# Optimization experiments

Measured on AMD Instinct MI355X. Metric: run time of the kernel, lower is better.

The kernel has to match this reference:

```python
import jax, jax.numpy as jnp
import numpy as np

H = 512
B = 32
T = 2048


def setup_inputs() -> dict:
    key = jax.random.key(0)
    ks = jax.random.split(key, 8)
    hidden = jax.random.normal(ks[0], (1, B, H), dtype=jnp.float32)
    encoder_outputs = jax.random.normal(ks[1], (T, B, H), dtype=jnp.float32)
    coverage = jax.random.uniform(ks[2], (B, T), dtype=jnp.float32)
    # nn.Linear(3H, H): weight [H, 3H], bias [H]
    W_attn = jax.random.normal(ks[3], (H, 3 * H), dtype=jnp.float32) / np.sqrt(3 * H)
    b_attn = jax.random.normal(ks[4], (H,), dtype=jnp.float32) / np.sqrt(3 * H)
    # v ~ Normal(0, 1/sqrt(H))
    v = jax.random.normal(ks[5], (H,), dtype=jnp.float32) / np.sqrt(H)
    # nn.Linear(1, H, bias=False): weight [H, 1]
    W_cov = jax.random.normal(ks[6], (H, 1), dtype=jnp.float32)
    return {"hidden": hidden, "encoder_outputs": encoder_outputs, "coverage": coverage,
            "W_attn": W_attn, "b_attn": b_attn, "v": v, "W_cov": W_cov}


def reference(hidden, encoder_outputs, coverage, W_attn, b_attn, v, W_cov):
    # hidden: [1,B,H], encoder_outputs: [T,B,H], coverage: [B,T]
    enc = jnp.transpose(encoder_outputs, (1, 0, 2))          # [B,T,H]
    b, t, h = enc.shape
    hrep = jnp.broadcast_to(hidden[0][:, None, :], (b, t, h))  # [B,T,H]
    # coverage_feature = Linear(1,H,bias=False)(coverage[...,None]) -> outer product
    cov_feat = coverage[..., None] * W_cov[:, 0]               # [B,T,H]
    x = jnp.concatenate([hrep, enc, cov_feat], axis=-1)        # [B,T,3H]
    energy = jax.nn.relu(jnp.einsum('btk,hk->bth', x, W_attn) + b_attn)  # [B,T,H]
    scores = jnp.einsum('bth,h->bt', energy, v)                # [B,T]
    attn_weights = jax.nn.softmax(scores, axis=1)              # softmax over T
    coverage_new = coverage + attn_weights                     # [B,T]
    return attn_weights[:, None, :], coverage_new
```

## Files before the change

### kernel.cpp

```cpp
#include <hip/hip_runtime.h>
#include <hip/hip_bf16.h>

typedef unsigned short u16;
typedef __attribute__((ext_vector_type(8))) short bf16x8;
typedef __attribute__((ext_vector_type(4))) float f32x4;

#define T_DIM 2048
#define B_DIM 32
#define H_DIM 512
#define M_DIM (T_DIM * B_DIM)

__device__ inline unsigned pack2(float a, float b) {
  union { __hip_bfloat162 h2; unsigned u; } c;
  c.h2 = __float22bfloat162_rn(make_float2(a, b));
  return c.u;
}

__global__ __launch_bounds__(256) void prep_kernel(
    const float* __restrict__ hidden, const float* __restrict__ W_attn,
    const float* __restrict__ b_attn, const float* __restrict__ W_cov,
    u16* __restrict__ W2bf, float* __restrict__ r, float* __restrict__ u)
{
  const int tid = blockIdx.x * 256 + threadIdx.x;
  const int pair = tid >> 2;
  const int kq = tid & 3;
  const int b = pair >> 9, h = pair & 511;

  {
    const float* hid = hidden + b * 512 + kq * 128;
    const float* w1 = W_attn + (size_t)h * 1536 + kq * 128;
    float acc = 0.f;
    #pragma unroll 8
    for (int k = 0; k < 128; k += 4) {
      float4 x = *(const float4*)(hid + k);
      float4 w = *(const float4*)(w1 + k);
      acc += x.x * w.x + x.y * w.y + x.z * w.z + x.w * w.w;
    }
    acc += __shfl_xor(acc, 1);
    acc += __shfl_xor(acc, 2);
    if (kq == 0) r[pair] = acc + b_attn[h];
  }

  {
    int j0 = tid * 4;
    int hh = j0 >> 9, kk = j0 & 511;
    float4 w = *(const float4*)(W_attn + (size_t)hh * 1536 + 512 + kk);
    uint2 p;
    p.x = pack2(w.x, w.y);
    p.y = pack2(w.z, w.w);
    int f = hh >> 4, c = hh & 15;
    int ks = kk >> 5, quad = (kk >> 3) & 3, e = kk & 7;
    *(uint2*)(W2bf + (size_t)((f * 16 + ks) * 64 + quad * 16 + c) * 8 + e) = p;
  }

  if (tid < 2048) {
    int h3 = tid >> 2;
    const float* w3 = W_attn + (size_t)h3 * 1536 + 1024 + kq * 128;
    const float* wc = W_cov + kq * 128;
    float su = 0.f;
    #pragma unroll 8
    for (int k = 0; k < 128; k += 4) {
      float4 a = *(const float4*)(w3 + k);
      float4 c = *(const float4*)(wc + k);
      su += a.x * c.x + a.y * c.y + a.z * c.z + a.w * c.w;
    }
    su += __shfl_xor(su, 1);
    su += __shfl_xor(su, 2);
    if (kq == 0) u[h3] = su;
  }
}

__global__ __launch_bounds__(512, 4) void gemm_score(
    const float* __restrict__ enc, const u16* __restrict__ W2bf,
    const float* __restrict__ r, const float* __restrict__ u,
    const float* __restrict__ vv, const float* __restrict__ cov,
    float* __restrict__ part)
{
  const int m0 = blockIdx.x * 64;
  const int tid = threadIdx.x;
  const int lane = tid & 63;
  const int w = tid >> 6;
  const int quad = lane >> 4, col = lane & 15;

  __shared__ u16 As[64 * 512];

  #pragma unroll
  for (int it = 0; it < 8; ++it) {
    int un = tid + 512 * it;
    int row = un >> 6;
    int g = un & 63;
    const float* ga = enc + (size_t)(m0 + row) * 512 + g * 8;
    float4 f0 = *(const float4*)ga;
    float4 f1 = *(const float4*)(ga + 4);
    uint4 p;
    p.x = pack2(f0.x, f0.y);
    p.y = pack2(f0.z, f0.w);
    p.z = pack2(f1.x, f1.y);
    p.w = pack2(f1.z, f1.w);
    *(uint4*)&As[row * 512 + (g ^ (row & 7)) * 8] = p;
  }
  __syncthreads();

  f32x4 acc[4][4] = {};
  const u16* bbase = W2bf + (size_t)w * 32768 + lane * 8;

  bf16x8 bcur[4], bnxt[4];
  #pragma unroll
  for (int j = 0; j < 4; ++j)
    bcur[j] = *(const bf16x8*)(bbase + j * 8192);

  #pragma unroll
  for (int ks = 0; ks < 16; ++ks) {
    if (ks < 15) {
      #pragma unroll
      for (int j = 0; j < 4; ++j)
        bnxt[j] = *(const bf16x8*)(bbase + j * 8192 + (ks + 1) * 512);
    }
    bf16x8 af[4];
    #pragma unroll
    for (int i = 0; i < 4; ++i) {
      int row = i * 16 + col;
      af[i] = *(const bf16x8*)&As[row * 512 + ((ks * 4 + quad) ^ (col & 7)) * 8];
    }
    #pragma unroll
    for (int i = 0; i < 4; ++i)
      #pragma unroll
      for (int j = 0; j < 4; ++j)
        acc[i][j] = __builtin_amdgcn_mfma_f32_16x16x32_bf16(af[i], bcur[j], acc[i][j], 0, 0, 0);
    #pragma unroll
    for (int j = 0; j < 4; ++j) bcur[j] = bnxt[j];
  }

  float uj[4], vj[4];
  #pragma unroll
  for (int j = 0; j < 4; ++j) {
    int gh = w * 64 + j * 16 + col;
    uj[j] = u[gh];
    vj[j] = vv[gh];
  }
  #pragma unroll
  for (int pair = 0; pair < 2; ++pair) {
    #pragma unroll
    for (int reg = 0; reg < 4; ++reg) {
      int b = pair * 16 + quad * 4 + reg;
      const float* rb = r + b * 512;
      float rbj[4];
      #pragma unroll
      for (int j = 0; j < 4; ++j) rbj[j] = rb[w * 64 + j * 16 + col];
      #pragma unroll
      for (int isub = 0; isub < 2; ++isub) {
        int i = pair + isub * 2;
        int t = (m0 >> 5) + isub;
        float cv = cov[b * 2048 + t];
        float s = 0.f;
        #pragma unroll
        for (int j = 0; j < 4; ++j) {
          float e = acc[i][j][reg] + rbj[j] + cv * uj[j];
          e = fmaxf(e, 0.f);
          s += e * vj[j];
        }
        s += __shfl_xor(s, 1);
        s += __shfl_xor(s, 2);
        s += __shfl_xor(s, 4);
        s += __shfl_xor(s, 8);
        if (col == 0) part[(size_t)(w * 32 + b) * 2048 + t] = s;
      }
    }
  }
}

__global__ __launch_bounds__(256) void softmax_kernel(
    const float* __restrict__ part, const float* __restrict__ cov, float* __restrict__ out)
{
  const int b = blockIdx.x;
  const int tid = threadIdx.x;
  const int lane = tid & 63, wid = tid >> 6;
  __shared__ float red[4];
  float loc[8];
  float lmax = -3.4e38f;
  #pragma unroll
  for (int i = 0; i < 8; ++i) {
    int t = tid + i * 256;
    float s = 0.f;
    #pragma unroll
    for (int p = 0; p < 8; ++p) s += part[(size_t)(p * 32 + b) * 2048 + t];
    loc[i] = s;
    lmax = fmaxf(lmax, s);
  }
  #pragma unroll
  for (int o = 32; o; o >>= 1) lmax = fmaxf(lmax, __shfl_xor(lmax, o));
  if (lane == 0) red[wid] = lmax;
  __syncthreads();
  float bmax = fmaxf(fmaxf(red[0], red[1]), fmaxf(red[2], red[3]));
  __syncthreads();
  float lsum = 0.f;
  #pragma unroll
  for (int i = 0; i < 8; ++i) { loc[i] = __expf(loc[i] - bmax); lsum += loc[i]; }
  #pragma unroll
  for (int o = 32; o; o >>= 1) lsum += __shfl_xor(lsum, o);
  if (lane == 0) red[wid] = lsum;
  __syncthreads();
  float inv = 1.0f / (red[0] + red[1] + red[2] + red[3]);
  #pragma unroll
  for (int i = 0; i < 8; ++i) {
    int t = tid + i * 256;
    float a = loc[i] * inv;
    out[b * 2048 + t] = a;
    out[65536 + b * 2048 + t] = cov[b * 2048 + t] + a;
  }
}

extern "C" void kernel_launch(void* const* d_in, const int* in_sizes, int n_in,
                              void* d_out, int out_size, void* d_ws, size_t ws_size,
                              hipStream_t stream) {
  const float* hidden = (const float*)d_in[0];
  const float* enc    = (const float*)d_in[1];
  const float* cov    = (const float*)d_in[2];
  const float* W_attn = (const float*)d_in[3];
  const float* b_attn = (const float*)d_in[4];
  const float* vv     = (const float*)d_in[5];
  const float* W_cov  = (const float*)d_in[6];
  float* out = (float*)d_out;

  u16* W2bf = (u16*)d_ws;
  float* r  = (float*)((char*)d_ws + 512 * 1024);
  float* u  = r + 32 * 512;
  float* part = u + 512;

  hipLaunchKernelGGL(prep_kernel, dim3(256), dim3(256), 0, stream,
                     hidden, W_attn, b_attn, W_cov, W2bf, r, u);
  hipLaunchKernelGGL(gemm_score, dim3(1024), dim3(512), 0, stream,
                     enc, W2bf, r, u, vv, cov, part);
  hipLaunchKernelGGL(softmax_kernel, dim3(32), dim3(256), 0, stream,
                     part, cov, out);
}
```

Baseline: 273.2 us.

## Stream fp32 encoder tiles into LDS asynchronously with double-buffered K chunks

Replaces the upfront synchronous load-and-convert of the whole 64x512 A tile with async global_load_lds copies of fp32 data. The copies go into two LDS buffers of 128-wide K chunks, so loading the next chunk overlaps MFMA work on the current one. The bf16 conversion moves from the staging step to each LDS read. Every one of the 8 waves now converts the same A fragments, which adds redundant VALU packing work. It also adds three extra block barriers.

```diff
diff --git a/kernel.cpp b/kernel.cpp
--- a/kernel.cpp
+++ b/kernel.cpp
@@ -2,6 +2,7 @@
 #include <hip/hip_bf16.h>
 
 typedef unsigned short u16;
+typedef unsigned int u32;
 typedef __attribute__((ext_vector_type(8))) short bf16x8;
 typedef __attribute__((ext_vector_type(4))) float f32x4;
 
@@ -14,6 +15,11 @@
   union { __hip_bfloat162 h2; unsigned u; } c;
   c.h2 = __float22bfloat162_rn(make_float2(a, b));
   return c.u;
+}
+
+__device__ inline void gload_lds16(const float* g, float* lds) {
+  __builtin_amdgcn_global_load_lds((const __attribute__((address_space(1))) u32*)g,
+                                   (__attribute__((address_space(3))) u32*)lds, 16, 0, 0);
 }
 
 __global__ __launch_bounds__(256) void prep_kernel(
@@ -82,53 +88,67 @@
   const int w = tid >> 6;
   const int quad = lane >> 4, col = lane & 15;
 
-  __shared__ u16 As[64 * 512];
-
-  #pragma unroll
-  for (int it = 0; it < 8; ++it) {
-    int un = tid + 512 * it;
-    int row = un >> 6;
-    int g = un & 63;
-    const float* ga = enc + (size_t)(m0 + row) * 512 + g * 8;
-    float4 f0 = *(const float4*)ga;
-    float4 f1 = *(const float4*)(ga + 4);
-    uint4 p;
-    p.x = pack2(f0.x, f0.y);
-    p.y = pack2(f0.z, f0.w);
-    p.z = pack2(f1.x, f1.y);
-    p.w = pack2(f1.z, f1.w);
-    *(uint4*)&As[row * 512 + (g ^ (row & 7)) * 8] = p;
-  }
-  __syncthreads();
+  __shared__ float As[2][64 * 128];
+
+  const int srow_half = lane >> 5;
+  const int sj = lane & 31;
 
   f32x4 acc[4][4] = {};
   const u16* bbase = W2bf + (size_t)w * 32768 + lane * 8;
 
-  bf16x8 bcur[4], bnxt[4];
+  #pragma unroll
+  for (int it = 0; it < 4; ++it) {
+    int c = w * 4 + it;
+    int row = 2 * c + srow_half;
+    int g = sj ^ (row & 7);
+    gload_lds16(enc + (size_t)(m0 + row) * 512 + 0 * 128 + g * 4, &As[0][c * 256]);
+  }
+  __syncthreads();
+
+  bf16x8 bbuf[2][4];
   #pragma unroll
   for (int j = 0; j < 4; ++j)
-    bcur[j] = *(const bf16x8*)(bbase + j * 8192);
-
-  #pragma unroll
-  for (int ks = 0; ks < 16; ++ks) {
-    if (ks < 15) {
-      #pragma unroll
-      for (int j = 0; j < 4; ++j)
-        bnxt[j] = *(const bf16x8*)(bbase + j * 8192 + (ks + 1) * 512);
-    }
-    bf16x8 af[4];
+    bbuf[0][j] = *(const bf16x8*)(bbase + j * 8192);
+
+  for (int q = 0; q < 4; ++q) {
+    if (q < 3) {
+      #pragma unroll
+      for (int it = 0; it < 4; ++it) {
+        int c = w * 4 + it;
+        int row = 2 * c + srow_half;
+        int g = sj ^ (row & 7);
+        gload_lds16(enc + (size_t)(m0 + row) * 512 + (q + 1) * 128 + g * 4,
+                    &As[(q + 1) & 1][c * 256]);
+      }
+    }
+    const float* Ab = As[q & 1];
     #pragma unroll
-    for (int i = 0; i < 4; ++i) {
-      int row = i * 16 + col;
-      af[i] = *(const bf16x8*)&As[row * 512 + ((ks * 4 + quad) ^ (col & 7)) * 8];
-    }
-    #pragma unroll
-    for (int i = 0; i < 4; ++i)
-      #pragma unroll
-      for (int j = 0; j < 4; ++j)
-        acc[i][j] = __builtin_amdgcn_mfma_f32_16x16x32_bf16(af[i], bcur[j], acc[i][j], 0, 0, 0);
-    #pragma unroll
-    for (int j = 0; j < 4; ++j) bcur[j] = bnxt[j];
+    for (int ksl = 0; ksl < 4; ++ksl) {
+      int ksg = q * 4 + ksl;
+      if (ksg < 15) {
+        #pragma unroll
+        for (int j = 0; j < 4; ++j)
+          bbuf[(ksg + 1) & 1][j] = *(const bf16x8*)(bbase + j * 8192 + (ksg + 1) * 512);
+      }
+      const int gb = ksl * 8 + quad * 2;
+      #pragma unroll
+      for (int i = 0; i < 4; ++i) {
+        int row = i * 16 + col;
+        int sw = col & 7;
+        float4 d0 = *(const float4*)&Ab[row * 128 + (gb ^ sw) * 4];
+        float4 d1 = *(const float4*)&Ab[row * 128 + ((gb + 1) ^ sw) * 4];
+        uint4 pa;
+        pa.x = pack2(d0.x, d0.y);
+        pa.y = pack2(d0.z, d0.w);
+        pa.z = pack2(d1.x, d1.y);
+        pa.w = pack2(d1.z, d1.w);
+        bf16x8 af = *(bf16x8*)&pa;
+        #pragma unroll
+        for (int j = 0; j < 4; ++j)
+          acc[i][j] = __builtin_amdgcn_mfma_f32_16x16x32_bf16(af, bbuf[ksg & 1][j], acc[i][j], 0, 0, 0);
+      }
+    }
+    if (q < 3) __syncthreads();
   }
 
   float uj[4], vj[4];
@@ -139,17 +159,17 @@
     vj[j] = vv[gh];
   }
   #pragma unroll
-  for (int pair = 0; pair < 2; ++pair) {
+  for (int pr = 0; pr < 2; ++pr) {
     #pragma unroll
     for (int reg = 0; reg < 4; ++reg) {
-      int b = pair * 16 + quad * 4 + reg;
+      int b = pr * 16 + quad * 4 + reg;
       const float* rb = r + b * 512;
       float rbj[4];
       #pragma unroll
       for (int j = 0; j < 4; ++j) rbj[j] = rb[w * 64 + j * 16 + col];
       #pragma unroll
       for (int isub = 0; isub < 2; ++isub) {
-        int i = pair + isub * 2;
+        int i = pr + isub * 2;
         int t = (m0 >> 5) + isub;
         float cv = cov[b * 2048 + t];
         float s = 0.f;
```

New measurement: 290.5 us. 1.06x slower.

## Load encoder tiles directly into registers, drop LDS staging, split N across blocks

Applied to the files above, without the earlier changes.

Removes the shared-memory staging of the fp32 encoder tile: each wave now loads its A fragments straight from global memory, converts them to bf16 in registers, and double-buffers both A and B loads across k-steps. The grid is doubled, with each 256-thread block covering half of the hidden dimension, so there are more, smaller blocks. This avoids the LDS write, the barrier and the LDS reads. In exchange, every wave re-reads encoder rows that other waves and the sibling block also read, using narrow strided accesses that depend on cache hits.

```diff
diff --git a/kernel.cpp b/kernel.cpp
--- a/kernel.cpp
+++ b/kernel.cpp
@@ -2,6 +2,7 @@
 #include <hip/hip_bf16.h>
 
 typedef unsigned short u16;
+typedef unsigned int u32;
 typedef __attribute__((ext_vector_type(8))) short bf16x8;
 typedef __attribute__((ext_vector_type(4))) float f32x4;
 
@@ -70,86 +71,85 @@
   }
 }
 
-__global__ __launch_bounds__(512, 4) void gemm_score(
+__global__ __launch_bounds__(256, 3) void gemm_score(
     const float* __restrict__ enc, const u16* __restrict__ W2bf,
     const float* __restrict__ r, const float* __restrict__ u,
     const float* __restrict__ vv, const float* __restrict__ cov,
     float* __restrict__ part)
 {
-  const int m0 = blockIdx.x * 64;
+  const int p = blockIdx.x;
+  const int m0 = (p & 1023) * 64;
+  const int y = p >> 10;
   const int tid = threadIdx.x;
   const int lane = tid & 63;
   const int w = tid >> 6;
+  const int slab = y * 4 + w;
   const int quad = lane >> 4, col = lane & 15;
 
-  __shared__ u16 As[64 * 512];
-
-  #pragma unroll
-  for (int it = 0; it < 8; ++it) {
-    int un = tid + 512 * it;
-    int row = un >> 6;
-    int g = un & 63;
-    const float* ga = enc + (size_t)(m0 + row) * 512 + g * 8;
-    float4 f0 = *(const float4*)ga;
-    float4 f1 = *(const float4*)(ga + 4);
-    uint4 p;
-    p.x = pack2(f0.x, f0.y);
-    p.y = pack2(f0.z, f0.w);
-    p.z = pack2(f1.x, f1.y);
-    p.w = pack2(f1.z, f1.w);
-    *(uint4*)&As[row * 512 + (g ^ (row & 7)) * 8] = p;
-  }
-  __syncthreads();
-
   f32x4 acc[4][4] = {};
-  const u16* bbase = W2bf + (size_t)w * 32768 + lane * 8;
-
-  bf16x8 bcur[4], bnxt[4];
+  const u16* bbase = W2bf + (size_t)(slab * 4) * 8192 + lane * 8;
+  const float* abase = enc + (size_t)(m0 + col) * 512 + quad * 8;
+
+  float4 araw[8];
+  bf16x8 bbuf[2][4];
+
+  #pragma unroll
+  for (int i = 0; i < 4; ++i) {
+    araw[i * 2]     = *(const float4*)(abase + i * 8192);
+    araw[i * 2 + 1] = *(const float4*)(abase + i * 8192 + 4);
+  }
   #pragma unroll
   for (int j = 0; j < 4; ++j)
-    bcur[j] = *(const bf16x8*)(bbase + j * 8192);
+    bbuf[0][j] = *(const bf16x8*)(bbase + j * 8192);
 
   #pragma unroll
   for (int ks = 0; ks < 16; ++ks) {
+    bf16x8 af[4];
+    #pragma unroll
+    for (int i = 0; i < 4; ++i) {
+      uint4 pa;
+      pa.x = pack2(araw[i * 2].x,     araw[i * 2].y);
+      pa.y = pack2(araw[i * 2].z,     araw[i * 2].w);
+      pa.z = pack2(araw[i * 2 + 1].x, araw[i * 2 + 1].y);
+      pa.w = pack2(araw[i * 2 + 1].z, araw[i * 2 + 1].w);
+      af[i] = *(bf16x8*)&pa;
+    }
     if (ks < 15) {
       #pragma unroll
+      for (int i = 0; i < 4; ++i) {
+        araw[i * 2]     = *(const float4*)(abase + i * 8192 + (ks + 1) * 32);
+        araw[i * 2 + 1] = *(const float4*)(abase + i * 8192 + (ks + 1) * 32 + 4);
+      }
+      #pragma unroll
       for (int j = 0; j < 4; ++j)
-        bnxt[j] = *(const bf16x8*)(bbase + j * 8192 + (ks + 1) * 512);
-    }
-    bf16x8 af[4];
-    #pragma unroll
-    for (int i = 0; i < 4; ++i) {
-      int row = i * 16 + col;
-      af[i] = *(const bf16x8*)&As[row * 512 + ((ks * 4 + quad) ^ (col & 7)) * 8];
+        bbuf[(ks + 1) & 1][j] = *(const bf16x8*)(bbase + j * 8192 + (ks + 1) * 512);
     }
     #pragma unroll
     for (int i = 0; i < 4; ++i)
       #pragma unroll
       for (int j = 0; j < 4; ++j)
-        acc[i][j] = __builtin_amdgcn_mfma_f32_16x16x32_bf16(af[i], bcur[j], acc[i][j], 0, 0, 0);
-    #pragma unroll
-    for (int j = 0; j < 4; ++j) bcur[j] = bnxt[j];
+        acc[i][j] = __builtin_amdgcn_mfma_f32_16x16x32_bf16(af[i], bbuf[ks & 1][j], acc[i][j], 0, 0, 0);
   }
 
   float uj[4], vj[4];
   #pragma unroll
   for (int j = 0; j < 4; ++j) {
-    int gh = w * 64 + j * 16 + col;
+    int gh = slab * 64 + j * 16 + col;
     uj[j] = u[gh];
     vj[j] = vv[gh];
   }
   #pragma unroll
-  for (int pair = 0; pair < 2; ++pair) {
+  for (int pr = 0; pr < 2; ++pr) {
     #pragma unroll
     for (int reg = 0; reg < 4; ++reg) {
-      int b = pair * 16 + quad * 4 + reg;
+      int b = pr * 16 + quad * 4 + reg;
       const float* rb = r + b * 512;
       float rbj[4];
       #pragma unroll
-      for (int j = 0; j < 4; ++j) rbj[j] = rb[w * 64 + j * 16 + col];
+      for (int j = 0; j < 4; ++j) rbj[j] = rb[slab * 64 + j * 16 + col];
       #pragma unroll
       for (int isub = 0; isub < 2; ++isub) {
-        int i = pair + isub * 2;
+        int i = pr + isub * 2;
         int t = (m0 >> 5) + isub;
         float cv = cov[b * 2048 + t];
         float s = 0.f;
@@ -163,7 +163,7 @@
         s += __shfl_xor(s, 2);
         s += __shfl_xor(s, 4);
         s += __shfl_xor(s, 8);
-        if (col == 0) part[(size_t)(w * 32 + b) * 2048 + t] = s;
+        if (col == 0) part[(size_t)(slab * 32 + b) * 2048 + t] = s;
       }
     }
   }
@@ -229,7 +229,7 @@
 
   hipLaunchKernelGGL(prep_kernel, dim3(256), dim3(256), 0, stream,
                      hidden, W_attn, b_attn, W_cov, W2bf, r, u);
-  hipLaunchKernelGGL(gemm_score, dim3(1024), dim3(512), 0, stream,
+  hipLaunchKernelGGL(gemm_score, dim3(2048), dim3(256), 0, stream,
                      enc, W2bf, r, u, vv, cov, part);
   hipLaunchKernelGGL(softmax_kernel, dim3(32), dim3(256), 0, stream,
                      part, cov, out);
```

Result: slower. 360.6 us (+32.0%).

## Pre-convert encoder outputs to swizzled bf16 and stream into LDS directly

Applied to the files above, without the earlier changes.

The fp32-to-bf16 conversion and swizzle of encoder_outputs move out of the GEMM kernel into an extended prep kernel. That kernel writes a pre-swizzled bf16 copy to a 64 MB workspace region. The GEMM then fills shared memory with global_load_lds direct-to-LDS copies, which avoids staging through registers and doing the conversion inside the compute kernel. The prep kernel is also restructured into block-specialised roles for conversion, r/u vectors and W2 packing, and the GEMM inner loop now double-buffers B fragments through an indexed array. The trade-off is an extra 64 MB write and reread of the encoder tensor, and a dependence on a larger workspace.

```diff
diff --git a/kernel.cpp b/kernel.cpp
--- a/kernel.cpp
+++ b/kernel.cpp
@@ -2,6 +2,7 @@
 #include <hip/hip_bf16.h>
 
 typedef unsigned short u16;
+typedef unsigned int u32;
 typedef __attribute__((ext_vector_type(8))) short bf16x8;
 typedef __attribute__((ext_vector_type(4))) float f32x4;
 
@@ -10,6 +11,10 @@
 #define H_DIM 512
 #define M_DIM (T_DIM * B_DIM)
 
+#define NCONV 4096
+#define NR 512
+#define NW2 256
+
 __device__ inline unsigned pack2(float a, float b) {
   union { __hip_bfloat162 h2; unsigned u; } c;
   c.h2 = __float22bfloat162_rn(make_float2(a, b));
@@ -17,31 +22,61 @@
 }
 
 __global__ __launch_bounds__(256) void prep_kernel(
-    const float* __restrict__ hidden, const float* __restrict__ W_attn,
-    const float* __restrict__ b_attn, const float* __restrict__ W_cov,
-    u16* __restrict__ W2bf, float* __restrict__ r, float* __restrict__ u)
+    const float* __restrict__ hidden, const float* __restrict__ enc,
+    const float* __restrict__ W_attn, const float* __restrict__ b_attn,
+    const float* __restrict__ W_cov,
+    u16* __restrict__ encbf, u16* __restrict__ W2bf,
+    float* __restrict__ r, float* __restrict__ u)
 {
-  const int tid = blockIdx.x * 256 + threadIdx.x;
-  const int pair = tid >> 2;
-  const int kq = tid & 3;
-  const int b = pair >> 9, h = pair & 511;
-
-  {
-    const float* hid = hidden + b * 512 + kq * 128;
-    const float* w1 = W_attn + (size_t)h * 1536 + kq * 128;
+  const int bid = blockIdx.x;
+  const int t = threadIdx.x;
+
+  if (bid < NCONV) {
+    #pragma unroll
+    for (int i = 0; i < 4; ++i) {
+      int o = bid * 1024 + i * 256 + t;
+      int mrow = o >> 6;
+      int gslot = o & 63;
+      int gd = gslot ^ (mrow & 7);
+      const float* src = enc + (size_t)mrow * 512 + gd * 8;
+      float4 f0 = *(const float4*)src;
+      float4 f1 = *(const float4*)(src + 4);
+      uint4 p;
+      p.x = pack2(f0.x, f0.y);
+      p.y = pack2(f0.z, f0.w);
+      p.z = pack2(f1.x, f1.y);
+      p.w = pack2(f1.z, f1.w);
+      *(uint4*)(encbf + (size_t)o * 8) = p;
+    }
+  } else if (bid < NCONV + NR) {
+    const int h = bid - NCONV;
+    const int bb = t >> 3, kq = t & 7;
+    const float* w1 = W_attn + (size_t)h * 1536 + kq * 64;
+    const float* hid = hidden + bb * 512 + kq * 64;
     float acc = 0.f;
-    #pragma unroll 8
-    for (int k = 0; k < 128; k += 4) {
+    #pragma unroll
+    for (int k = 0; k < 64; k += 4) {
       float4 x = *(const float4*)(hid + k);
-      float4 w = *(const float4*)(w1 + k);
-      acc += x.x * w.x + x.y * w.y + x.z * w.z + x.w * w.w;
+      float4 ww = *(const float4*)(w1 + k);
+      acc += x.x * ww.x + x.y * ww.y + x.z * ww.z + x.w * ww.w;
     }
     acc += __shfl_xor(acc, 1);
     acc += __shfl_xor(acc, 2);
-    if (kq == 0) r[pair] = acc + b_attn[h];
-  }
-
-  {
+    acc += __shfl_xor(acc, 4);
+    if (kq == 0) r[bb * 512 + h] = acc + b_attn[h];
+    if (t < 64) {
+      const float* w3 = W_attn + (size_t)h * 1536 + 1024 + t * 8;
+      const float* wc = W_cov + t * 8;
+      float4 a0 = *(const float4*)w3, a1 = *(const float4*)(w3 + 4);
+      float4 c0 = *(const float4*)wc, c1 = *(const float4*)(wc + 4);
+      float su = a0.x * c0.x + a0.y * c0.y + a0.z * c0.z + a0.w * c0.w
+               + a1.x * c1.x + a1.y * c1.y + a1.z * c1.z + a1.w * c1.w;
+      #pragma unroll
+      for (int o = 32; o; o >>= 1) su += __shfl_xor(su, o);
+      if (t == 0) u[h] = su;
+    }
+  } else {
+    const int tid = (bid - NCONV - NR) * 256 + t;
     int j0 = tid * 4;
     int hh = j0 >> 9, kk = j0 & 511;
     float4 w = *(const float4*)(W_attn + (size_t)hh * 1536 + 512 + kk);
@@ -52,31 +87,16 @@
     int ks = kk >> 5, quad = (kk >> 3) & 3, e = kk & 7;
     *(uint2*)(W2bf + (size_t)((f * 16 + ks) * 64 + quad * 16 + c) * 8 + e) = p;
   }
-
-  if (tid < 2048) {
-    int h3 = tid >> 2;
-    const float* w3 = W_attn + (size_t)h3 * 1536 + 1024 + kq * 128;
-    const float* wc = W_cov + kq * 128;
-    float su = 0.f;
-    #pragma unroll 8
-    for (int k = 0; k < 128; k += 4) {
-      float4 a = *(const float4*)(w3 + k);
-      float4 c = *(const float4*)(wc + k);
-      su += a.x * c.x + a.y * c.y + a.z * c.z + a.w * c.w;
-    }
-    su += __shfl_xor(su, 1);
-    su += __shfl_xor(su, 2);
-    if (kq == 0) u[h3] = su;
-  }
 }
 
 __global__ __launch_bounds__(512, 4) void gemm_score(
-    const float* __restrict__ enc, const u16* __restrict__ W2bf,
+    const u16* __restrict__ encbf, const u16* __restrict__ W2bf,
     const float* __restrict__ r, const float* __restrict__ u,
     const float* __restrict__ vv, const float* __restrict__ cov,
     float* __restrict__ part)
 {
-  const int m0 = blockIdx.x * 64;
+  const int mt = blockIdx.x;
+  const int m0 = mt * 64;
   const int tid = threadIdx.x;
   const int lane = tid & 63;
   const int w = tid >> 6;
@@ -84,51 +104,41 @@
 
   __shared__ u16 As[64 * 512];
 
-  #pragma unroll
-  for (int it = 0; it < 8; ++it) {
-    int un = tid + 512 * it;
-    int row = un >> 6;
-    int g = un & 63;
-    const float* ga = enc + (size_t)(m0 + row) * 512 + g * 8;
-    float4 f0 = *(const float4*)ga;
-    float4 f1 = *(const float4*)(ga + 4);
-    uint4 p;
-    p.x = pack2(f0.x, f0.y);
-    p.y = pack2(f0.z, f0.w);
-    p.z = pack2(f1.x, f1.y);
-    p.w = pack2(f1.z, f1.w);
-    *(uint4*)&As[row * 512 + (g ^ (row & 7)) * 8] = p;
+  {
+    const u16* g = encbf + ((size_t)mt * 4096 + w * 64 + lane) * 8;
+    #pragma unroll
+    for (int it = 0; it < 8; ++it) {
+      __builtin_amdgcn_global_load_lds(
+          (const __attribute__((address_space(1))) u32*)(g + (size_t)it * 512 * 8),
+          (__attribute__((address_space(3))) u32*)(As + (it * 512 + w * 64) * 8),
+          16, 0, 0);
+    }
   }
   __syncthreads();
 
   f32x4 acc[4][4] = {};
   const u16* bbase = W2bf + (size_t)w * 32768 + lane * 8;
 
-  bf16x8 bcur[4], bnxt[4];
+  bf16x8 bbuf[2][4];
   #pragma unroll
   for (int j = 0; j < 4; ++j)
-    bcur[j] = *(const bf16x8*)(bbase + j * 8192);
+    bbuf[0][j] = *(const bf16x8*)(bbase + j * 8192);
 
   #pragma unroll
   for (int ks = 0; ks < 16; ++ks) {
     if (ks < 15) {
       #pragma unroll
       for (int j = 0; j < 4; ++j)
-        bnxt[j] = *(const bf16x8*)(bbase + j * 8192 + (ks + 1) * 512);
-    }
-    bf16x8 af[4];
+        bbuf[(ks + 1) & 1][j] = *(const bf16x8*)(bbase + j * 8192 + (ks + 1) * 512);
+    }
     #pragma unroll
     for (int i = 0; i < 4; ++i) {
       int row = i * 16 + col;
-      af[i] = *(const bf16x8*)&As[row * 512 + ((ks * 4 + quad) ^ (col & 7)) * 8];
-    }
-    #pragma unroll
-    for (int i = 0; i < 4; ++i)
+      bf16x8 af = *(const bf16x8*)&As[row * 512 + ((ks * 4 + quad) ^ (col & 7)) * 8];
       #pragma unroll
       for (int j = 0; j < 4; ++j)
-        acc[i][j] = __builtin_amdgcn_mfma_f32_16x16x32_bf16(af[i], bcur[j], acc[i][j], 0, 0, 0);
-    #pragma unroll
-    for (int j = 0; j < 4; ++j) bcur[j] = bnxt[j];
+        acc[i][j] = __builtin_amdgcn_mfma_f32_16x16x32_bf16(af, bbuf[ks & 1][j], acc[i][j], 0, 0, 0);
+    }
   }
 
   float uj[4], vj[4];
@@ -139,17 +149,17 @@
     vj[j] = vv[gh];
   }
   #pragma unroll
-  for (int pair = 0; pair < 2; ++pair) {
+  for (int pr = 0; pr < 2; ++pr) {
     #pragma unroll
     for (int reg = 0; reg < 4; ++reg) {
-      int b = pair * 16 + quad * 4 + reg;
+      int b = pr * 16 + quad * 4 + reg;
       const float* rb = r + b * 512;
       float rbj[4];
       #pragma unroll
       for (int j = 0; j < 4; ++j) rbj[j] = rb[w * 64 + j * 16 + col];
       #pragma unroll
       for (int isub = 0; isub < 2; ++isub) {
-        int i = pair + isub * 2;
+        int i = pr + isub * 2;
         int t = (m0 >> 5) + isub;
         float cv = cov[b * 2048 + t];
         float s = 0.f;
@@ -222,15 +232,16 @@
   const float* W_cov  = (const float*)d_in[6];
   float* out = (float*)d_out;
 
-  u16* W2bf = (u16*)d_ws;
-  float* r  = (float*)((char*)d_ws + 512 * 1024);
-  float* u  = r + 32 * 512;
+  u16* encbf = (u16*)d_ws;
+  u16* W2bf  = (u16*)((char*)d_ws + (size_t)67108864);
+  float* r   = (float*)((char*)d_ws + 67108864 + 524288);
+  float* u   = r + 32 * 512;
   float* part = u + 512;
 
-  hipLaunchKernelGGL(prep_kernel, dim3(256), dim3(256), 0, stream,
-                     hidden, W_attn, b_attn, W_cov, W2bf, r, u);
+  hipLaunchKernelGGL(prep_kernel, dim3(NCONV + NR + NW2), dim3(256), 0, stream,
+                     hidden, enc, W_attn, b_attn, W_cov, encbf, W2bf, r, u);
   hipLaunchKernelGGL(gemm_score, dim3(1024), dim3(512), 0, stream,
-                     enc, W2bf, r, u, vv, cov, part);
+                     encbf, W2bf, r, u, vv, cov, part);
   hipLaunchKernelGGL(softmax_kernel, dim3(32), dim3(256), 0, stream,
                      part, cov, out);
 }
```

Measured after the change: 284.6 us. 1.04x slower.
